# Kernel tuning notes

Measured on AMD Instinct MI355X. Metric: run time of the kernel, lower is better.

The kernel has to match this reference:

```python
import math
import jax, jax.numpy as jnp
import numpy as np

B, S, H, N = 2, 2048, 2048, 16
HN = H // N
ALPHA = 32.0
MASK_VALUE = 10000.0


def setup_inputs() -> dict:
    key = jax.random.key(0)
    k1, k2, k3, k4, k5 = jax.random.split(key, 5)
    hidden_states = jax.random.normal(k1, (B, S, H), dtype=jnp.float32)
    # causal (left-to-right) multiplicative mask, broadcastable to [b, n, s, s]
    ltor_mask = jnp.tril(jnp.ones((S, S), dtype=jnp.float32))[None, None, :, :]
    # torch Linear params: y = x @ W.T + b
    w_qkv = jax.random.normal(k2, (3 * H, H), dtype=jnp.float32) * (1.0 / math.sqrt(H))
    b_qkv = jnp.zeros((3 * H,), dtype=jnp.float32)
    w_dense = jax.random.normal(k3, (H, H), dtype=jnp.float32) * (1.0 / math.sqrt(H))
    b_dense = jnp.zeros((H,), dtype=jnp.float32)
    return {"hidden_states": hidden_states, "ltor_mask": ltor_mask,
            "w_qkv": w_qkv, "b_qkv": b_qkv, "w_dense": w_dense, "b_dense": b_dense}


def reference(hidden_states, ltor_mask, w_qkv, b_qkv, w_dense, b_dense):
    b, s, h = hidden_states.shape
    # fused qkv projection
    qkv = hidden_states @ w_qkv.T + b_qkv                       # [b, s, 3h]
    q, k, v = jnp.split(qkv, 3, axis=-1)

    def heads(t):  # [b, s, h] -> [b, n, s, hn]
        return t.reshape(b, s, N, HN).transpose(0, 2, 1, 3)

    q, k, v = heads(q), heads(k), heads(v)
    # cogview pb_relax: scale query before matmul
    scores = jnp.einsum('bnsd,bntd->bnst', q / math.sqrt(HN), k)  # [b, n, s, s]
    m = ltor_mask[:, :, -s:]
    scores = scores * m - MASK_VALUE * (1.0 - m)
    # pb_relax max stabilization: per (batch, head) global max of scores/alpha
    scaled = scores / ALPHA
    maxes = jax.lax.stop_gradient(jnp.max(scaled, axis=(-2, -1), keepdims=True))
    scores = (scaled - maxes) * ALPHA
    probs = jax.nn.softmax(scores, axis=-1)
    ctx = jnp.einsum('bnst,bntd->bnsd', probs, v)                # [b, n, s, hn]
    ctx = ctx.transpose(0, 2, 1, 3).reshape(b, s, h)
    out = ctx @ w_dense.T + b_dense
    return out
```

## Files before the change

kernel.cpp:

```cpp
#include <hip/hip_runtime.h>

typedef __bf16 bf16_t;
typedef __bf16 bf16x8 __attribute__((ext_vector_type(8)));
typedef __bf16 bf16x4 __attribute__((ext_vector_type(4)));
typedef float f32x4 __attribute__((ext_vector_type(4)));

#define MFMA16(a, b, c) __builtin_amdgcn_mfma_f32_16x16x32_bf16((a), (b), (c), 0, 0, 0)

__device__ __forceinline__ void gload_lds16(const void* g, void* l) {
  __builtin_amdgcn_global_load_lds(
      (__attribute__((address_space(1))) void*)(g),
      (__attribute__((address_space(3))) void*)(l), 16, 0, 0);
}

__device__ __forceinline__ void block_bar() {
  asm volatile("" ::: "memory");
  __builtin_amdgcn_s_barrier();
  asm volatile("" ::: "memory");
}

__global__ __launch_bounds__(256) void cvt_f32_bf16(const float* __restrict__ in,
                                                    bf16_t* __restrict__ out, int n4) {
  int i = blockIdx.x * 256 + threadIdx.x;
  if (i >= n4) return;
  float4 v = ((const float4*)in)[i];
  bf16x4 o;
  o[0] = (bf16_t)v.x; o[1] = (bf16_t)v.y; o[2] = (bf16_t)v.z; o[3] = (bf16_t)v.w;
  ((bf16x4*)out)[i] = o;
}

__global__ __launch_bounds__(512) void gemm_qkv_256(
    const bf16_t* __restrict__ A, const bf16_t* __restrict__ Bw,
    const float* __restrict__ bias,
    bf16_t* __restrict__ qb, bf16_t* __restrict__ kb, bf16_t* __restrict__ vtb,
    int M, int N, int K) {
  __shared__ __attribute__((aligned(16))) bf16_t As[3][256][32];
  __shared__ __attribute__((aligned(16))) bf16_t Bs[3][256][32];
  const int tid = threadIdx.x;
  const int lane = tid & 63;
  const int w = tid >> 6;
  const int wm = w >> 2, wn = w & 3;
  const int l15 = lane & 15, l4 = lane >> 4;
  const int bm = blockIdx.y * 256, bn = blockIdx.x * 256;

  f32x4 acc[8][4];
#pragma unroll
  for (int i = 0; i < 8; ++i)
#pragma unroll
    for (int j = 0; j < 4; ++j)
#pragma unroll
      for (int r = 0; r < 4; ++r) acc[i][j][r] = 0.0f;

  const int srow = tid >> 2;
  const int schk = tid & 3;

  auto stageA = [&](int q, int ti, int i) {
    int r = (i << 7) + srow;
    int cl = (schk ^ (r & 3)) << 3;
    gload_lds16(A + (size_t)(bm + r) * K + (ti << 5) + cl, &As[q][r][schk << 3]);
  };
  auto stageB = [&](int q, int ti, int i) {
    int r = (i << 7) + srow;
    int cl = (schk ^ (r & 3)) << 3;
    gload_lds16(Bw + (size_t)(bn + r) * K + (ti << 5) + cl, &Bs[q][r][schk << 3]);
  };
  auto afrag = [&](int p, int mf) -> bf16x8 {
    int row = wm * 128 + mf * 16 + l15;
    int ch = l4 ^ (row & 3);
    return *(const bf16x8*)(&As[p][row][ch << 3]);
  };
  auto bfrag = [&](int p, int nf) -> bf16x8 {
    int row = wn * 64 + nf * 16 + l15;
    int ch = l4 ^ (row & 3);
    return *(const bf16x8*)(&Bs[p][row][ch << 3]);
  };

  const int nt = K >> 5;

#pragma unroll
  for (int i = 0; i < 2; ++i) stageA(0, 0, i);
#pragma unroll
  for (int i = 0; i < 2; ++i) stageB(0, 0, i);
#pragma unroll
  for (int i = 0; i < 2; ++i) stageA(1, 1, i);
#pragma unroll
  for (int i = 0; i < 2; ++i) stageB(1, 1, i);

#pragma unroll 1
  for (int t = 0; t < nt; ++t) {
    const int sl = t % 3;
    if (t + 1 < nt) {
      asm volatile("s_waitcnt vmcnt(4)" ::: "memory");
    } else {
      asm volatile("s_waitcnt vmcnt(0)" ::: "memory");
    }
    block_bar();

    const bool pf = (t + 2 < nt);
    const int s2 = pf ? (t + 2) % 3 : 0;

    bf16x8 bfr[4], afr[4];
#pragma unroll
    for (int n = 0; n < 4; ++n) bfr[n] = bfrag(sl, n);
#pragma unroll
    for (int j = 0; j < 4; ++j) afr[j] = afrag(sl, j);
    if (pf) { stageA(s2, t + 2, 0); stageA(s2, t + 2, 1); }
    __builtin_amdgcn_s_setprio(1);
#pragma unroll
    for (int j = 0; j < 4; ++j)
#pragma unroll
      for (int n = 0; n < 4; ++n) acc[j][n] = MFMA16(afr[j], bfr[n], acc[j][n]);
    __builtin_amdgcn_s_setprio(0);

#pragma unroll
    for (int j = 0; j < 4; ++j) afr[j] = afrag(sl, 4 + j);
    if (pf) { stageB(s2, t + 2, 0); stageB(s2, t + 2, 1); }
    __builtin_amdgcn_s_setprio(1);
#pragma unroll
    for (int j = 0; j < 4; ++j)
#pragma unroll
      for (int n = 0; n < 4; ++n) acc[4 + j][n] = MFMA16(afr[j], bfr[n], acc[4 + j][n]);
    __builtin_amdgcn_s_setprio(0);
    block_bar();
  }

  const int which = bn >> 11;
#pragma unroll
  for (int mf = 0; mf < 8; ++mf)
#pragma unroll
    for (int nf = 0; nf < 4; ++nf)
#pragma unroll
      for (int r = 0; r < 4; ++r) {
        int m = bm + wm * 128 + mf * 16 + l4 * 4 + r;
        int n = bn + wn * 64 + nf * 16 + l15;
        float v = acc[mf][nf][r] + bias[n];
        int b = m >> 11, s = m & 2047;
        int d = n & 127;
        int head = (n & 2047) >> 7;
        size_t hb = (size_t)(b * 16 + head);
        if (which == 0) {
          v *= 0.08838834764831845f;
          qb[(hb * 2048 + s) * 128 + d] = (bf16_t)v;
        } else if (which == 1) {
          kb[(hb * 2048 + s) * 128 + d] = (bf16_t)v;
        } else {
          vtb[(hb * 128 + d) * 2048 + s] = (bf16_t)v;
        }
      }
}

__global__ __launch_bounds__(256) void gemm_bt_dense(
    const bf16_t* __restrict__ A, const bf16_t* __restrict__ Bw,
    const float* __restrict__ bias, float* __restrict__ O,
    int M, int N, int K) {
  __shared__ __attribute__((aligned(16))) bf16_t As[2][128][32];
  __shared__ __attribute__((aligned(16))) bf16_t Bs[2][128][32];
  const int tid = threadIdx.x;
  const int lane = tid & 63, wave = tid >> 6;
  const int wr = (wave >> 1) * 64, wc = (wave & 1) * 64;
  const int l15 = lane & 15, l4 = lane >> 4;
  const int bm = blockIdx.y * 128, bn = blockIdx.x * 128;

  f32x4 acc[4][4];
#pragma unroll
  for (int i = 0; i < 4; ++i)
#pragma unroll
    for (int j = 0; j < 4; ++j)
#pragma unroll
      for (int r = 0; r < 4; ++r) acc[i][j][r] = 0.0f;

  const int r0 = tid >> 2;
  const int co = (tid & 3) * 8;
  const bf16_t* gA = A + (size_t)(bm + r0) * K + co;
  const bf16_t* gB = Bw + (size_t)(bn + r0) * K + co;

  const int nt = K >> 5;

  gload_lds16(gA, &As[0][r0][co]);
  gload_lds16(gA + (size_t)64 * K, &As[0][r0 + 64][co]);
  gload_lds16(gB, &Bs[0][r0][co]);
  gload_lds16(gB + (size_t)64 * K, &Bs[0][r0 + 64][co]);

#pragma unroll 1
  for (int t = 0; t < nt; ++t) {
    const int cb = t & 1;
    if (t + 1 < nt) {
      const int kk = (t + 1) << 5;
      const int nb = cb ^ 1;
      gload_lds16(gA + kk, &As[nb][r0][co]);
      gload_lds16(gA + kk + (size_t)64 * K, &As[nb][r0 + 64][co]);
      gload_lds16(gB + kk, &Bs[nb][r0][co]);
      gload_lds16(gB + kk + (size_t)64 * K, &Bs[nb][r0 + 64][co]);
      asm volatile("s_waitcnt vmcnt(4)" ::: "memory");
    } else {
      asm volatile("s_waitcnt vmcnt(0)" ::: "memory");
    }
    block_bar();
    bf16x8 a[4], b[4];
#pragma unroll
    for (int i = 0; i < 4; ++i) a[i] = *(const bf16x8*)(&As[cb][wr + i * 16 + l15][l4 * 8]);
#pragma unroll
    for (int j = 0; j < 4; ++j) b[j] = *(const bf16x8*)(&Bs[cb][wc + j * 16 + l15][l4 * 8]);
#pragma unroll
    for (int i = 0; i < 4; ++i)
#pragma unroll
      for (int j = 0; j < 4; ++j) acc[i][j] = MFMA16(a[i], b[j], acc[i][j]);
    block_bar();
  }

#pragma unroll
  for (int i = 0; i < 4; ++i)
#pragma unroll
    for (int j = 0; j < 4; ++j)
#pragma unroll
      for (int r = 0; r < 4; ++r) {
        int m = bm + wr + i * 16 + l4 * 4 + r;
        int n = bn + wc + j * 16 + l15;
        O[(size_t)m * N + n] = acc[i][j][r] + bias[n];
      }
}

__global__ __launch_bounds__(512) void attn_kernel(
    const bf16_t* __restrict__ qbuf, const bf16_t* __restrict__ kbuf,
    const bf16_t* __restrict__ vtbuf, bf16_t* __restrict__ ctx) {
  __shared__ __attribute__((aligned(16))) bf16_t Ks[2][64][128];
  __shared__ __attribute__((aligned(16))) bf16_t Vts[2][128][64];
  __shared__ __attribute__((aligned(16))) bf16_t Ps[8][16][64];

  const int tid = threadIdx.x, lane = tid & 63, w = tid >> 6;
  const int l15 = lane & 15, l4 = lane >> 4;
  const int hb = blockIdx.y;
  const size_t hoff = (size_t)hb * 2048 * 128;
  const bf16_t* qh = qbuf + hoff;
  const bf16_t* kh = kbuf + hoff;
  const bf16_t* vh = vtbuf + hoff;
  const int b = hb >> 4, head = hb & 15;

  const int kr0 = tid >> 4, ks0 = tid & 15;
  const int vr0 = tid >> 3, vs0 = tid & 7;

  int buf = 0;

#pragma unroll 1
  for (int phase = 0; phase < 2; ++phase) {
    const int qt = phase == 0 ? blockIdx.x : 15 - blockIdx.x;
    const int q0 = qt * 128;
    const int nt = 2 * qt + 2;

    bf16x8 qa[4];
#pragma unroll
    for (int ks = 0; ks < 4; ++ks)
      qa[ks] = *(const bf16x8*)(qh + (size_t)(q0 + w * 16 + l15) * 128 + ks * 32 + l4 * 8);

    f32x4 accO[8];
#pragma unroll
    for (int df = 0; df < 8; ++df)
#pragma unroll
      for (int r = 0; r < 4; ++r) accO[df][r] = 0.0f;
    float mrow[4], lrow[4];
#pragma unroll
    for (int r = 0; r < 4; ++r) { mrow[r] = -1e30f; lrow[r] = 0.0f; }

    {
      const int kv0 = 0;
#pragma unroll
      for (int it = 0; it < 2; ++it) {
        int row = kr0 + it * 32, sch = ks0 ^ (row & 7);
        gload_lds16(kh + (size_t)(kv0 + row) * 128 + sch * 8, &Ks[buf][row][ks0 * 8]);
      }
#pragma unroll
      for (int it = 0; it < 2; ++it) {
        int row = vr0 + it * 64, sch = vs0 ^ (row & 7);
        gload_lds16(vh + (size_t)row * 2048 + kv0 + sch * 8, &Vts[buf][row][vs0 * 8]);
      }
    }

#pragma unroll 1
    for (int t = 0; t < nt; ++t) {
      const int kv0 = t * 64;
      if (t + 1 < nt) {
        const int kvn = (t + 1) * 64;
        const int nb = buf ^ 1;
#pragma unroll
        for (int it = 0; it < 2; ++it) {
          int row = kr0 + it * 32, sch = ks0 ^ (row & 7);
          gload_lds16(kh + (size_t)(kvn + row) * 128 + sch * 8, &Ks[nb][row][ks0 * 8]);
        }
#pragma unroll
        for (int it = 0; it < 2; ++it) {
          int row = vr0 + it * 64, sch = vs0 ^ (row & 7);
          gload_lds16(vh + (size_t)row * 2048 + kvn + sch * 8, &Vts[nb][row][vs0 * 8]);
        }
        asm volatile("s_waitcnt vmcnt(4)" ::: "memory");
      } else {
        asm volatile("s_waitcnt vmcnt(0)" ::: "memory");
      }
      block_bar();

      const bool active = (kv0 <= q0 + w * 16 + 15);
      if (active) {
        f32x4 sc[4];
#pragma unroll
        for (int nf = 0; nf < 4; ++nf) {
#pragma unroll
          for (int r = 0; r < 4; ++r) sc[nf][r] = 0.0f;
          int row = nf * 16 + l15;
#pragma unroll
          for (int ks = 0; ks < 4; ++ks) {
            int ch = (ks * 4 + l4) ^ (row & 7);
            bf16x8 kf = *(const bf16x8*)(&Ks[buf][row][ch * 8]);
            sc[nf] = MFMA16(qa[ks], kf, sc[nf]);
          }
        }

        if (kv0 + 63 > q0 + w * 16) {
#pragma unroll
          for (int nf = 0; nf < 4; ++nf)
#pragma unroll
            for (int r = 0; r < 4; ++r) {
              int qi = q0 + w * 16 + l4 * 4 + r;
              int kv = kv0 + nf * 16 + l15;
              if (kv > qi) sc[nf][r] = -1e30f;
            }
        }

        float tmax[4];
#pragma unroll
        for (int r = 0; r < 4; ++r)
          tmax[r] = fmaxf(fmaxf(sc[0][r], sc[1][r]), fmaxf(sc[2][r], sc[3][r]));
#pragma unroll
        for (int msk = 1; msk <= 8; msk <<= 1)
#pragma unroll
          for (int r = 0; r < 4; ++r)
            tmax[r] = fmaxf(tmax[r], __shfl_xor(tmax[r], msk, 64));

        bool defer = __all(tmax[0] <= mrow[0] + 8.0f && tmax[1] <= mrow[1] + 8.0f &&
                           tmax[2] <= mrow[2] + 8.0f && tmax[3] <= mrow[3] + 8.0f);
        if (!defer) {
          float scl[4];
#pragma unroll
          for (int r = 0; r < 4; ++r) {
            float mn = fmaxf(mrow[r], tmax[r]);
            scl[r] = __expf(mrow[r] - mn);
            mrow[r] = mn;
            lrow[r] *= scl[r];
          }
#pragma unroll
          for (int df = 0; df < 8; ++df)
#pragma unroll
            for (int r = 0; r < 4; ++r) accO[df][r] *= scl[r];
        }

        float rsum[4];
#pragma unroll
        for (int r = 0; r < 4; ++r) {
          float s0 = 0.0f;
#pragma unroll
          for (int nf = 0; nf < 4; ++nf) {
            float p = __expf(sc[nf][r] - mrow[r]);
            sc[nf][r] = p;
            s0 += p;
          }
          rsum[r] = s0;
        }
#pragma unroll
        for (int msk = 1; msk <= 8; msk <<= 1)
#pragma unroll
          for (int r = 0; r < 4; ++r) rsum[r] += __shfl_xor(rsum[r], msk, 64);
#pragma unroll
        for (int r = 0; r < 4; ++r) lrow[r] += rsum[r];

#pragma unroll
        for (int nf = 0; nf < 4; ++nf)
#pragma unroll
          for (int r = 0; r < 4; ++r) {
            int qi = l4 * 4 + r;
            int kv = nf * 16 + l15;
            int ch = (kv >> 3) ^ (qi & 7);
            Ps[w][qi][ch * 8 + (kv & 7)] = (bf16_t)sc[nf][r];
          }

        bf16x8 pa[2];
#pragma unroll
        for (int k2 = 0; k2 < 2; ++k2) {
          int ch = (k2 * 4 + l4) ^ (l15 & 7);
          pa[k2] = *(const bf16x8*)(&Ps[w][l15][ch * 8]);
        }
#pragma unroll
        for (int df = 0; df < 8; ++df) {
          int row = df * 16 + l15;
#pragma unroll
          for (int k2 = 0; k2 < 2; ++k2) {
            int ch = (k2 * 4 + l4) ^ (row & 7);
            bf16x8 vf = *(const bf16x8*)(&Vts[buf][row][ch * 8]);
            accO[df] = MFMA16(pa[k2], vf, accO[df]);
          }
        }
      }
      block_bar();
      buf ^= 1;
    }

    float inv[4];
#pragma unroll
    for (int r = 0; r < 4; ++r) inv[r] = 1.0f / lrow[r];
#pragma unroll
    for (int df = 0; df < 8; ++df)
#pragma unroll
      for (int r = 0; r < 4; ++r) {
        int s = q0 + w * 16 + l4 * 4 + r;
        int col = head * 128 + df * 16 + l15;
        ctx[((size_t)(b * 2048 + s)) * 2048 + col] = (bf16_t)(accO[df][r] * inv[r]);
      }
  }
}

extern "C" void kernel_launch(void* const* d_in, const int* in_sizes, int n_in,
                              void* d_out, int out_size, void* d_ws, size_t ws_size,
                              hipStream_t stream) {
  const float* hs = (const float*)d_in[0];
  const float* w_qkv = (const float*)d_in[2];
  const float* b_qkv = (const float*)d_in[3];
  const float* w_dense = (const float*)d_in[4];
  const float* b_dense = (const float*)d_in[5];
  float* out = (float*)d_out;

  const size_t SZ_HS = (size_t)4096 * 2048;
  const size_t SZ_WQKV = (size_t)6144 * 2048;
  const size_t SZ_WD = (size_t)2048 * 2048;
  const size_t SZ_H = (size_t)32 * 2048 * 128;

  char* ws = (char*)d_ws;
  bf16_t* A_ = (bf16_t*)ws;
  bf16_t* B_ = (bf16_t*)(ws + 2 * SZ_HS);
  bf16_t* Q_ = (bf16_t*)(ws + 2 * (SZ_HS + SZ_WQKV));
  bf16_t* K_ = Q_ + SZ_H;
  bf16_t* V_ = K_ + SZ_H;

  cvt_f32_bf16<<<(int)(SZ_HS / 4 / 256), 256, 0, stream>>>(hs, A_, (int)(SZ_HS / 4));
  cvt_f32_bf16<<<(int)(SZ_WQKV / 4 / 256), 256, 0, stream>>>(w_qkv, B_, (int)(SZ_WQKV / 4));

  gemm_qkv_256<<<dim3(24, 16), 512, 0, stream>>>(A_, B_, b_qkv, Q_, K_, V_, 4096, 6144, 2048);

  cvt_f32_bf16<<<(int)(SZ_WD / 4 / 256), 256, 0, stream>>>(w_dense, A_, (int)(SZ_WD / 4));

  attn_kernel<<<dim3(8, 32), 512, 0, stream>>>(Q_, K_, V_, B_);

  gemm_bt_dense<<<dim3(16, 32), 256, 0, stream>>>(B_, A_, b_dense, out, 4096, 2048, 2048);
}
```

Measured before the change: 431.4 us.

## Repack QKV GEMM LDS layout, add fourth stage buffer and intra-iteration barriers

```diff
diff --git a/kernel.cpp b/kernel.cpp
--- a/kernel.cpp
+++ b/kernel.cpp
@@ -34,8 +34,8 @@
     const float* __restrict__ bias,
     bf16_t* __restrict__ qb, bf16_t* __restrict__ kb, bf16_t* __restrict__ vtb,
     int M, int N, int K) {
-  __shared__ __attribute__((aligned(16))) bf16_t As[3][256][32];
-  __shared__ __attribute__((aligned(16))) bf16_t Bs[3][256][32];
+  __shared__ __attribute__((aligned(16))) bf16_t As[4][256][32];
+  __shared__ __attribute__((aligned(16))) bf16_t Bs[4][256][32];
   const int tid = threadIdx.x;
   const int lane = tid & 63;
   const int w = tid >> 6;
@@ -51,28 +51,30 @@
 #pragma unroll
       for (int r = 0; r < 4; ++r) acc[i][j][r] = 0.0f;
 
-  const int srow = tid >> 2;
-  const int schk = tid & 3;
-
-  auto stageA = [&](int q, int ti, int i) {
-    int r = (i << 7) + srow;
-    int cl = (schk ^ (r & 3)) << 3;
-    gload_lds16(A + (size_t)(bm + r) * K + (ti << 5) + cl, &As[q][r][schk << 3]);
+  const int srow_lo = ((tid >> 3) << 1) + ((tid >> 2) & 1);
+  const int schk = (tid & 3) ^ ((tid >> 3) & 3);
+
+  auto stageA = [&](int sl, int ti, int i) {
+    int row = (i << 7) + srow_lo;
+    gload_lds16(A + (size_t)(bm + row) * K + (ti << 5) + (schk << 3),
+                (bf16_t*)As[sl] + i * 4096 + tid * 8);
   };
-  auto stageB = [&](int q, int ti, int i) {
-    int r = (i << 7) + srow;
-    int cl = (schk ^ (r & 3)) << 3;
-    gload_lds16(Bw + (size_t)(bn + r) * K + (ti << 5) + cl, &Bs[q][r][schk << 3]);
+  auto stageB = [&](int sl, int ti, int i) {
+    int row = (i << 7) + srow_lo;
+    gload_lds16(Bw + (size_t)(bn + row) * K + (ti << 5) + (schk << 3),
+                (bf16_t*)Bs[sl] + i * 4096 + tid * 8);
   };
-  auto afrag = [&](int p, int mf) -> bf16x8 {
+  auto afrag = [&](int sl, int mf) -> bf16x8 {
     int row = wm * 128 + mf * 16 + l15;
-    int ch = l4 ^ (row & 3);
-    return *(const bf16x8*)(&As[p][row][ch << 3]);
+    int line = row >> 1;
+    int off = line * 64 + (((row & 1) << 2) + (l4 ^ (line & 3))) * 8;
+    return *(const bf16x8*)((const bf16_t*)As[sl] + off);
   };
-  auto bfrag = [&](int p, int nf) -> bf16x8 {
+  auto bfrag = [&](int sl, int nf) -> bf16x8 {
     int row = wn * 64 + nf * 16 + l15;
-    int ch = l4 ^ (row & 3);
-    return *(const bf16x8*)(&Bs[p][row][ch << 3]);
+    int line = row >> 1;
+    int off = line * 64 + (((row & 1) << 2) + (l4 ^ (line & 3))) * 8;
+    return *(const bf16x8*)((const bf16_t*)Bs[sl] + off);
   };
 
   const int nt = K >> 5;
@@ -85,10 +87,15 @@
   for (int i = 0; i < 2; ++i) stageA(1, 1, i);
 #pragma unroll
   for (int i = 0; i < 2; ++i) stageB(1, 1, i);
+
+  bf16x8 afr[4], bfr[4];
 
 #pragma unroll 1
   for (int t = 0; t < nt; ++t) {
-    const int sl = t % 3;
+    const int sl = t & 3;
+    const bool pf = (t + 2 < nt);
+    const int s2 = (t + 2) & 3;
+
     if (t + 1 < nt) {
       asm volatile("s_waitcnt vmcnt(4)" ::: "memory");
     } else {
@@ -96,25 +103,24 @@
     }
     block_bar();
 
-    const bool pf = (t + 2 < nt);
-    const int s2 = pf ? (t + 2) % 3 : 0;
-
-    bf16x8 bfr[4], afr[4];
 #pragma unroll
     for (int n = 0; n < 4; ++n) bfr[n] = bfrag(sl, n);
 #pragma unroll
     for (int j = 0; j < 4; ++j) afr[j] = afrag(sl, j);
     if (pf) { stageA(s2, t + 2, 0); stageA(s2, t + 2, 1); }
+    block_bar();
     __builtin_amdgcn_s_setprio(1);
 #pragma unroll
     for (int j = 0; j < 4; ++j)
 #pragma unroll
       for (int n = 0; n < 4; ++n) acc[j][n] = MFMA16(afr[j], bfr[n], acc[j][n]);
     __builtin_amdgcn_s_setprio(0);
+    block_bar();
 
 #pragma unroll
     for (int j = 0; j < 4; ++j) afr[j] = afrag(sl, 4 + j);
     if (pf) { stageB(s2, t + 2, 0); stageB(s2, t + 2, 1); }
+    block_bar();
     __builtin_amdgcn_s_setprio(1);
 #pragma unroll
     for (int j = 0; j < 4; ++j)
```

After: 438.1 us. No clear change (+1.6%).
